# Kernel optimization log

Hardware: AMD Instinct MI355X
Metric: run time of the kernel (lower is better)

Reference implementation:

```python
import jax, jax.numpy as jnp
import numpy as np

N = 16384          # number of units
K = 655
BOOST_STRENGTH = 1.0


def setup_inputs() -> dict:
    key = jax.random.key(0)
    k1, k2 = jax.random.split(key)
    x = jax.random.normal(k1, (4096, N), dtype=jnp.float32)
    dutyCycle = jax.random.uniform(k2, (N,), dtype=jnp.float32)
    return {"x": x, "dutyCycle": dutyCycle}


def reference(x, dutyCycle):
    # boost factor per unit: encourages under-used units
    targetDensity = K / x.shape[1]
    boostFactors = jnp.exp((targetDensity - dutyCycle) * BOOST_STRENGTH)  # (N,)
    boosted = x * boostFactors  # (B, N)
    # top-k per row, then scatter a binary mask of winners
    _, idx = jax.lax.top_k(boosted, K)  # (B, K)
    b = jnp.arange(x.shape[0])[:, None]  # (B, 1)
    res = jnp.zeros_like(x).at[b, idx].set(1.0)
    return res
```

## Files before the change

kernel.cpp:

```cpp
#include <hip/hip_runtime.h>
#include <math.h>
#include <stdint.h>


#define N_UNITS 16384
#define K_WIN 655
#define NT 512
#define NPROBE 11
#define CAP 2048

__device__ __forceinline__ uint32_t fkey(float f) {
    uint32_t b = __float_as_uint(f);
    uint32_t m = (uint32_t)((int32_t)b >> 31) | 0x80000000u;
    return b ^ m;
}

__global__ void boost_kernel(const float* __restrict__ duty,
                             float* __restrict__ bf, int n) {
    int i = blockIdx.x * blockDim.x + threadIdx.x;
    if (i < n) {
        const float td = 0.03997802734375f;
        float s = td - duty[i];
        bf[i] = (float)exp((double)s);
    }
}

__global__ __launch_bounds__(NT, 6) void kwinners_kernel(
    const float* __restrict__ x, const float* __restrict__ bf,
    float* __restrict__ out) {
    __shared__ __align__(16) uint32_t khiw[N_UNITS / 2];
    __shared__ uint32_t red[(NT / 64) * NPROBE];
    __shared__ int cglob[NPROBE];
    __shared__ uint32_t cand_idx[CAP];
    __shared__ uint32_t cand_key[CAP];
    __shared__ int prb[NPROBE];
    __shared__ int sc[2];

    const int tid = threadIdx.x;
    const int lane = tid & 63;
    const int w = tid >> 6;
    const int row = blockIdx.x;
    const float4* xrow = (const float4*)(x + (size_t)row * N_UNITS);
    const float4* bfv = (const float4*)bf;
    float* orow = out + (size_t)row * N_UNITS;

    if (tid < NPROBE) {
        const float pv[NPROBE] = {1.90f, 1.70f, 1.55f, 1.43f, 1.33f, 1.25f,
                                  1.18f, 1.12f, 1.06f, 0.99f, 0.90f};
        prb[tid] = (int)(fkey(pv[tid]) >> 16);
    }
    if (tid == 0) sc[0] = 0;
    __syncthreads();

    int P[NPROBE];
#pragma unroll
    for (int p = 0; p < NPROBE; ++p) P[p] = prb[p];
    int cnt[NPROBE];
#pragma unroll
    for (int p = 0; p < NPROBE; ++p) cnt[p] = 0;

#pragma unroll
    for (int j = 0; j < N_UNITS / (NT * 4); ++j) {
        int i4 = tid + j * NT;
        float4 xv = xrow[i4];
        float4 bv = bfv[i4];
        int h0 = (int)(fkey(xv.x * bv.x) >> 16);
        int h1 = (int)(fkey(xv.y * bv.y) >> 16);
        int h2 = (int)(fkey(xv.z * bv.z) >> 16);
        int h3 = (int)(fkey(xv.w * bv.w) >> 16);
        uint2 pk;
        pk.x = (uint32_t)h0 | ((uint32_t)h1 << 16);
        pk.y = (uint32_t)h2 | ((uint32_t)h3 << 16);
        ((uint2*)khiw)[i4] = pk;
#pragma unroll
        for (int p = 0; p < NPROBE; ++p)
            cnt[p] += (h0 > P[p]) + (h1 > P[p]) + (h2 > P[p]) + (h3 > P[p]);
    }

    auto reduce_counts = [&]() {
#pragma unroll
        for (int p = 0; p < NPROBE; ++p) {
            int v = cnt[p];
#pragma unroll
            for (int m = 32; m >= 1; m >>= 1) v += __shfl_xor(v, m, 64);
            if (lane == 0) red[w * NPROBE + p] = (uint32_t)v;
        }
        __syncthreads();
        if (tid < NPROBE) {
            int s = 0;
#pragma unroll
            for (int ww = 0; ww < NT / 64; ++ww) s += (int)red[ww * NPROBE + tid];
            cglob[tid] = s;
        }
        __syncthreads();
    };
    reduce_counts();

    int lo, hi, cab, cgl;
    {
        int j = 0;
        while (j < NPROBE && cglob[j] < K_WIN) ++j;
        if (j == 0) {
            lo = P[0]; cgl = cglob[0]; hi = 65535; cab = 0;
        } else if (j == NPROBE) {
            lo = -1; cgl = N_UNITS; hi = P[NPROBE - 1]; cab = cglob[NPROBE - 1];
        } else {
            lo = P[j]; cgl = cglob[j]; hi = P[j - 1]; cab = cglob[j - 1];
        }
    }
    int m = cgl - cab;

    while (m > CAP && (hi - lo) > 1) {
        __syncthreads();
        if (tid < NPROBE)
            prb[tid] = lo + (int)(((long)(hi - lo) * (NPROBE - tid)) / (NPROBE + 1));
        __syncthreads();
#pragma unroll
        for (int p = 0; p < NPROBE; ++p) P[p] = prb[p];
#pragma unroll
        for (int p = 0; p < NPROBE; ++p) cnt[p] = 0;
        for (int j = 0; j < 4; ++j) {
            uint4 wv = ((const uint4*)khiw)[tid + j * NT];
            int h0 = (int)(wv.x & 0xFFFFu), h1 = (int)(wv.x >> 16);
            int h2 = (int)(wv.y & 0xFFFFu), h3 = (int)(wv.y >> 16);
            int h4 = (int)(wv.z & 0xFFFFu), h5 = (int)(wv.z >> 16);
            int h6 = (int)(wv.w & 0xFFFFu), h7 = (int)(wv.w >> 16);
#pragma unroll
            for (int p = 0; p < NPROBE; ++p)
                cnt[p] += (h0 > P[p]) + (h1 > P[p]) + (h2 > P[p]) + (h3 > P[p]) +
                          (h4 > P[p]) + (h5 > P[p]) + (h6 > P[p]) + (h7 > P[p]);
        }
        reduce_counts();
        int j = 0;
        while (j < NPROBE && cglob[j] < K_WIN) ++j;
        if (j == 0) {
            lo = P[0]; cgl = cglob[0];
        } else if (j == NPROBE) {
            hi = P[NPROBE - 1]; cab = cglob[NPROBE - 1];
        } else {
            lo = P[j]; cgl = cglob[j]; hi = P[j - 1]; cab = cglob[j - 1];
        }
        m = cgl - cab;
    }

    for (int j = 0; j < 4; ++j) {
        int q = tid + j * NT;
        uint4 wv = ((const uint4*)khiw)[q];
        int base = q * 8;
        int h[8] = {(int)(wv.x & 0xFFFFu), (int)(wv.x >> 16),
                    (int)(wv.y & 0xFFFFu), (int)(wv.y >> 16),
                    (int)(wv.z & 0xFFFFu), (int)(wv.z >> 16),
                    (int)(wv.w & 0xFFFFu), (int)(wv.w >> 16)};
#pragma unroll
        for (int e = 0; e < 8; ++e) {
            if (h[e] > lo && h[e] <= hi) {
                int p = atomicAdd(&sc[0], 1);
                if (p < CAP) cand_idx[p] = (uint32_t)(base + e);
            }
        }
    }
    __syncthreads();
    const int mm = sc[0];
    const int need = K_WIN - cab;

    const float* xr = x + (size_t)row * N_UNITS;
    const int mc = (mm <= CAP) ? mm : 0;
    for (int j = tid; j < mc; j += NT) {
        int i = (int)cand_idx[j];
        cand_key[j] = fkey(xr[i] * bf[i]);
    }

    for (int j = 0; j < N_UNITS / (NT * 4); ++j) {
        int f = tid + j * NT;
        uint2 wv = ((const uint2*)khiw)[f];
        float4 o;
        o.x = ((int)(wv.x & 0xFFFFu) > hi) ? 1.0f : 0.0f;
        o.y = ((int)(wv.x >> 16) > hi) ? 1.0f : 0.0f;
        o.z = ((int)(wv.y & 0xFFFFu) > hi) ? 1.0f : 0.0f;
        o.w = ((int)(wv.y >> 16) > hi) ? 1.0f : 0.0f;
        ((float4*)orow)[f] = o;
    }
    __syncthreads();

    if (mm <= CAP) {
        for (int j = tid; j < mm; j += NT) {
            uint32_t myk = cand_key[j];
            uint32_t myi = cand_idx[j];
            int r = 0;
            for (int l = 0; l < mm; ++l) {
                uint32_t lk = cand_key[l];
                r += (lk > myk) || (lk == myk && cand_idx[l] < myi);
            }
            if (r < need) orow[myi] = 1.0f;
        }
    } else if (tid == 0) {
        uint32_t* h8 = cand_idx;
        for (int b = 0; b < 256; ++b) h8[b] = 0;
        for (int i = 0; i < N_UNITS; ++i) {
            int h = (int)((khiw[i >> 1] >> ((i & 1) * 16)) & 0xFFFFu);
            if (h == hi) h8[(fkey(xr[i] * bf[i]) & 0xFFFFu) >> 8]++;
        }
        int acc = 0, d1 = 0, need2 = 0;
        for (int b = 255; b >= 0; --b) {
            int c = (int)h8[b];
            if (acc + c >= need) { d1 = b; need2 = need - acc; break; }
            acc += c;
        }
        for (int b = 0; b < 256; ++b) h8[b] = 0;
        for (int i = 0; i < N_UNITS; ++i) {
            int h = (int)((khiw[i >> 1] >> ((i & 1) * 16)) & 0xFFFFu);
            if (h == hi) {
                uint32_t kl = fkey(xr[i] * bf[i]) & 0xFFFFu;
                if ((int)(kl >> 8) == d1) h8[kl & 0xFFu]++;
            }
        }
        int acc2 = 0, d2 = 0, need3 = 0;
        for (int b = 255; b >= 0; --b) {
            int c = (int)h8[b];
            if (acc2 + c >= need2) { d2 = b; need3 = need2 - acc2; break; }
            acc2 += c;
        }
        uint32_t Tlo = ((uint32_t)d1 << 8) | (uint32_t)d2;
        int r = 0;
        for (int i = 0; i < N_UNITS; ++i) {
            int h = (int)((khiw[i >> 1] >> ((i & 1) * 16)) & 0xFFFFu);
            if (h == hi) {
                uint32_t kl = fkey(xr[i] * bf[i]) & 0xFFFFu;
                if (kl > Tlo) orow[i] = 1.0f;
                else if (kl == Tlo && r < need3) { orow[i] = 1.0f; ++r; }
            }
        }
    }
}

extern "C" void kernel_launch(void* const* d_in, const int* in_sizes, int n_in,
                              void* d_out, int out_size, void* d_ws,
                              size_t ws_size, hipStream_t stream) {
    const float* x = (const float*)d_in[0];
    const float* duty = (const float*)d_in[1];
    float* out = (float*)d_out;
    float* bf = (float*)d_ws;

    hipLaunchKernelGGL(boost_kernel, dim3(N_UNITS / 256), dim3(256), 0, stream,
                       duty, bf, N_UNITS);
    int rows = out_size / N_UNITS;
    hipLaunchKernelGGL(kwinners_kernel, dim3(rows), dim3(NT), 0, stream, x, bf,
                       out);
}
```

Measured before the change: 454.1 us.

## Keep 16-bit key prefixes in registers and count probes with wave ballots

Removes the 32KB shared-memory array of packed key prefixes and keeps each thread's eight packed words in registers across the probe, refinement and candidate passes. Per-probe counts now come from wave-wide ballot+popcount, so every lane holds the wave total and the shuffle reduction goes away. The output mask write is fused into the candidate-collection loop. The aim is to cut LDS traffic and LDS footprint so more blocks fit per CU, at the cost of extra register pressure, more ballot instructions, and a slow fallback path that recomputes keys from global memory.

Result: slower. 503.2 us (+10.8%).

```diff
diff --git a/kernel.cpp b/kernel.cpp
--- a/kernel.cpp
+++ b/kernel.cpp
@@ -8,6 +8,7 @@
 #define NT 512
 #define NPROBE 11
 #define CAP 2048
+#define ITERS (N_UNITS / (NT * 4))
 
 __device__ __forceinline__ uint32_t fkey(float f) {
     uint32_t b = __float_as_uint(f);
@@ -28,13 +29,12 @@
 __global__ __launch_bounds__(NT, 6) void kwinners_kernel(
     const float* __restrict__ x, const float* __restrict__ bf,
     float* __restrict__ out) {
-    __shared__ __align__(16) uint32_t khiw[N_UNITS / 2];
     __shared__ uint32_t red[(NT / 64) * NPROBE];
     __shared__ int cglob[NPROBE];
+    __shared__ int prb[NPROBE];
     __shared__ uint32_t cand_idx[CAP];
     __shared__ uint32_t cand_key[CAP];
-    __shared__ int prb[NPROBE];
-    __shared__ int sc[2];
+    __shared__ int sc[1];
 
     const int tid = threadIdx.x;
     const int lane = tid & 63;
@@ -44,23 +44,24 @@
     const float4* bfv = (const float4*)bf;
     float* orow = out + (size_t)row * N_UNITS;
 
-    if (tid < NPROBE) {
+    if (tid == 0) sc[0] = 0;
+
+    int P[NPROBE];
+    {
         const float pv[NPROBE] = {1.90f, 1.70f, 1.55f, 1.43f, 1.33f, 1.25f,
                                   1.18f, 1.12f, 1.06f, 0.99f, 0.90f};
-        prb[tid] = (int)(fkey(pv[tid]) >> 16);
-    }
-    if (tid == 0) sc[0] = 0;
-    __syncthreads();
-
-    int P[NPROBE];
-#pragma unroll
-    for (int p = 0; p < NPROBE; ++p) P[p] = prb[p];
+#pragma unroll
+        for (int p = 0; p < NPROBE; ++p) P[p] = (int)(fkey(pv[p]) >> 16);
+    }
+
     int cnt[NPROBE];
 #pragma unroll
     for (int p = 0; p < NPROBE; ++p) cnt[p] = 0;
 
-#pragma unroll
-    for (int j = 0; j < N_UNITS / (NT * 4); ++j) {
+    uint2 kh[ITERS];
+
+#pragma unroll
+    for (int j = 0; j < ITERS; ++j) {
         int i4 = tid + j * NT;
         float4 xv = xrow[i4];
         float4 bv = bfv[i4];
@@ -68,22 +69,21 @@
         int h1 = (int)(fkey(xv.y * bv.y) >> 16);
         int h2 = (int)(fkey(xv.z * bv.z) >> 16);
         int h3 = (int)(fkey(xv.w * bv.w) >> 16);
-        uint2 pk;
-        pk.x = (uint32_t)h0 | ((uint32_t)h1 << 16);
-        pk.y = (uint32_t)h2 | ((uint32_t)h3 << 16);
-        ((uint2*)khiw)[i4] = pk;
+        kh[j].x = (uint32_t)h0 | ((uint32_t)h1 << 16);
+        kh[j].y = (uint32_t)h2 | ((uint32_t)h3 << 16);
 #pragma unroll
         for (int p = 0; p < NPROBE; ++p)
-            cnt[p] += (h0 > P[p]) + (h1 > P[p]) + (h2 > P[p]) + (h3 > P[p]);
+            cnt[p] += __popcll(__ballot(h0 > P[p])) +
+                      __popcll(__ballot(h1 > P[p])) +
+                      __popcll(__ballot(h2 > P[p])) +
+                      __popcll(__ballot(h3 > P[p]));
     }
 
     auto reduce_counts = [&]() {
-#pragma unroll
-        for (int p = 0; p < NPROBE; ++p) {
-            int v = cnt[p];
-#pragma unroll
-            for (int m = 32; m >= 1; m >>= 1) v += __shfl_xor(v, m, 64);
-            if (lane == 0) red[w * NPROBE + p] = (uint32_t)v;
+        if (lane == 0) {
+#pragma unroll
+            for (int p = 0; p < NPROBE; ++p)
+                red[w * NPROBE + p] = (uint32_t)cnt[p];
         }
         __syncthreads();
         if (tid < NPROBE) {
@@ -119,16 +119,16 @@
         for (int p = 0; p < NPROBE; ++p) P[p] = prb[p];
 #pragma unroll
         for (int p = 0; p < NPROBE; ++p) cnt[p] = 0;
-        for (int j = 0; j < 4; ++j) {
-            uint4 wv = ((const uint4*)khiw)[tid + j * NT];
-            int h0 = (int)(wv.x & 0xFFFFu), h1 = (int)(wv.x >> 16);
-            int h2 = (int)(wv.y & 0xFFFFu), h3 = (int)(wv.y >> 16);
-            int h4 = (int)(wv.z & 0xFFFFu), h5 = (int)(wv.z >> 16);
-            int h6 = (int)(wv.w & 0xFFFFu), h7 = (int)(wv.w >> 16);
+#pragma unroll
+        for (int j = 0; j < ITERS; ++j) {
+            int h0 = (int)(kh[j].x & 0xFFFFu), h1 = (int)(kh[j].x >> 16);
+            int h2 = (int)(kh[j].y & 0xFFFFu), h3 = (int)(kh[j].y >> 16);
 #pragma unroll
             for (int p = 0; p < NPROBE; ++p)
-                cnt[p] += (h0 > P[p]) + (h1 > P[p]) + (h2 > P[p]) + (h3 > P[p]) +
-                          (h4 > P[p]) + (h5 > P[p]) + (h6 > P[p]) + (h7 > P[p]);
+                cnt[p] += __popcll(__ballot(h0 > P[p])) +
+                          __popcll(__ballot(h1 > P[p])) +
+                          __popcll(__ballot(h2 > P[p])) +
+                          __popcll(__ballot(h3 > P[p]));
         }
         reduce_counts();
         int j = 0;
@@ -143,16 +143,21 @@
         m = cgl - cab;
     }
 
-    for (int j = 0; j < 4; ++j) {
-        int q = tid + j * NT;
-        uint4 wv = ((const uint4*)khiw)[q];
-        int base = q * 8;
-        int h[8] = {(int)(wv.x & 0xFFFFu), (int)(wv.x >> 16),
-                    (int)(wv.y & 0xFFFFu), (int)(wv.y >> 16),
-                    (int)(wv.z & 0xFFFFu), (int)(wv.z >> 16),
-                    (int)(wv.w & 0xFFFFu), (int)(wv.w >> 16)};
-#pragma unroll
-        for (int e = 0; e < 8; ++e) {
+#pragma unroll
+    for (int j = 0; j < ITERS; ++j) {
+        int f = tid + j * NT;
+        int h0 = (int)(kh[j].x & 0xFFFFu), h1 = (int)(kh[j].x >> 16);
+        int h2 = (int)(kh[j].y & 0xFFFFu), h3 = (int)(kh[j].y >> 16);
+        float4 o;
+        o.x = (h0 > hi) ? 1.0f : 0.0f;
+        o.y = (h1 > hi) ? 1.0f : 0.0f;
+        o.z = (h2 > hi) ? 1.0f : 0.0f;
+        o.w = (h3 > hi) ? 1.0f : 0.0f;
+        ((float4*)orow)[f] = o;
+        int base = f * 4;
+        int h[4] = {h0, h1, h2, h3};
+#pragma unroll
+        for (int e = 0; e < 4; ++e) {
             if (h[e] > lo && h[e] <= hi) {
                 int p = atomicAdd(&sc[0], 1);
                 if (p < CAP) cand_idx[p] = (uint32_t)(base + e);
@@ -168,17 +173,6 @@
     for (int j = tid; j < mc; j += NT) {
         int i = (int)cand_idx[j];
         cand_key[j] = fkey(xr[i] * bf[i]);
-    }
-
-    for (int j = 0; j < N_UNITS / (NT * 4); ++j) {
-        int f = tid + j * NT;
-        uint2 wv = ((const uint2*)khiw)[f];
-        float4 o;
-        o.x = ((int)(wv.x & 0xFFFFu) > hi) ? 1.0f : 0.0f;
-        o.y = ((int)(wv.x >> 16) > hi) ? 1.0f : 0.0f;
-        o.z = ((int)(wv.y & 0xFFFFu) > hi) ? 1.0f : 0.0f;
-        o.w = ((int)(wv.y >> 16) > hi) ? 1.0f : 0.0f;
-        ((float4*)orow)[f] = o;
     }
     __syncthreads();
 
@@ -197,8 +191,8 @@
         uint32_t* h8 = cand_idx;
         for (int b = 0; b < 256; ++b) h8[b] = 0;
         for (int i = 0; i < N_UNITS; ++i) {
-            int h = (int)((khiw[i >> 1] >> ((i & 1) * 16)) & 0xFFFFu);
-            if (h == hi) h8[(fkey(xr[i] * bf[i]) & 0xFFFFu) >> 8]++;
+            uint32_t kf = fkey(xr[i] * bf[i]);
+            if ((int)(kf >> 16) == hi) h8[(kf & 0xFFFFu) >> 8]++;
         }
         int acc = 0, d1 = 0, need2 = 0;
         for (int b = 255; b >= 0; --b) {
@@ -208,11 +202,9 @@
         }
         for (int b = 0; b < 256; ++b) h8[b] = 0;
         for (int i = 0; i < N_UNITS; ++i) {
-            int h = (int)((khiw[i >> 1] >> ((i & 1) * 16)) & 0xFFFFu);
-            if (h == hi) {
-                uint32_t kl = fkey(xr[i] * bf[i]) & 0xFFFFu;
-                if ((int)(kl >> 8) == d1) h8[kl & 0xFFu]++;
-            }
+            uint32_t kf = fkey(xr[i] * bf[i]);
+            if ((int)(kf >> 16) == hi && (int)((kf & 0xFFFFu) >> 8) == d1)
+                h8[kf & 0xFFu]++;
         }
         int acc2 = 0, d2 = 0, need3 = 0;
         for (int b = 255; b >= 0; --b) {
@@ -223,9 +215,9 @@
         uint32_t Tlo = ((uint32_t)d1 << 8) | (uint32_t)d2;
         int r = 0;
         for (int i = 0; i < N_UNITS; ++i) {
-            int h = (int)((khiw[i >> 1] >> ((i & 1) * 16)) & 0xFFFFu);
-            if (h == hi) {
-                uint32_t kl = fkey(xr[i] * bf[i]) & 0xFFFFu;
+            uint32_t kf = fkey(xr[i] * bf[i]);
+            if ((int)(kf >> 16) == hi) {
+                uint32_t kl = kf & 0xFFFFu;
                 if (kl > Tlo) orow[i] = 1.0f;
                 else if (kl == Tlo && r < need3) { orow[i] = 1.0f; ++r; }
             }
```
